# Kernel tuning notes

Hardware: AMD Instinct MI355X
Metric: run time of the kernel (lower is better)

Reference implementation:

```python
import jax, jax.numpy as jnp
import numpy as np

NUM_EXPERTS = 8

def setup_inputs() -> dict:
    key = jax.random.key(0)
    k1, k2, k3, k4, k5 = jax.random.split(key, 5)
    B, T, E, C = 4, 4096, NUM_EXPERTS, 512
    in_features, out_features = 1024, 4096
    i = in_features // E
    x = jax.random.normal(k1, (B, T, E, i), dtype=jnp.float32)
    weight = jax.random.normal(k2, (out_features, in_features), dtype=jnp.float32) * 0.02
    bias = jax.random.normal(k3, (out_features,), dtype=jnp.float32) * 0.02
    combine_array = jax.random.uniform(k4, (B, T, E, C), dtype=jnp.float32)
    dispatch_mask = jax.random.uniform(k5, (B, T, E, C), dtype=jnp.float32)
    return {"x": x, "weight": weight, "bias": bias,
            "combine_array": combine_array, "dispatch_mask": dispatch_mask}

def reference(x, weight, bias, combine_array, dispatch_mask):
    E = NUM_EXPERTS
    expert_in = weight.shape[1] // E
    # (O, E*i) -> (E, O, i), matching torch's weight.reshape(E, -1, i)
    w = weight.reshape(E, -1, expert_in)
    B = x.shape[0]
    xr = x.reshape(B, -1, E, expert_in)  # (B, T, E, i)
    # dispatch: gather tokens into per-expert buffers (B, E, C, i)
    xd = jnp.einsum('btei,btec->beci', xr, dispatch_mask)
    # homogeneous coords to fold bias into the per-expert matmul
    x_h = jnp.concatenate([xd, jnp.ones_like(xd[..., :1])], axis=-1)           # (B,E,C,i+1)
    b_h = jnp.broadcast_to(bias.reshape(1, -1, 1), (E, w.shape[1], 1))
    w_h = jnp.concatenate([w, b_h], axis=-1)                                    # (E,O,i+1)
    # per-expert grouped GEMM, then scatter-combine back to tokens
    y = jnp.einsum('beci,eoi->beco', x_h, w_h)                                  # (B,E,C,O)
    out = jnp.einsum('beco,btec->bto', y, combine_array)                        # (B,T,O)
    return out
```

## Files before the change

### kernel.cpp

```cpp
#include <hip/hip_runtime.h>
#include <hip/hip_bf16.h>

typedef short sx8 __attribute__((ext_vector_type(8)));
typedef short sx4 __attribute__((ext_vector_type(4)));
typedef float f32x4 __attribute__((ext_vector_type(4)));

__device__ __forceinline__ short f2bf(float f) {
  union { float f; unsigned u; } v; v.f = f;
  unsigned r = v.u + 0x7fffu + ((v.u >> 16) & 1u);
  return (short)(r >> 16);
}

#define GLL16(g, l)                                          \
  __builtin_amdgcn_global_load_lds(                          \
      (__attribute__((address_space(1))) void*)(g),          \
      (__attribute__((address_space(3))) void*)(l), 16, 0, 0)

__global__ __launch_bounds__(256) void w2t_kernel(const float* __restrict__ w,
                                                  short* __restrict__ W2T) {
  const long idx = (long)blockIdx.x * 256 + threadIdx.x;
  const int o = (int)(idx >> 10);
  const int r = (int)(idx & 1023);
  W2T[idx] = f2bf(w[((long)((r >> 7) * 4096 + o) << 7) + (r & 127)]);
}

__global__ __launch_bounds__(256) void tr_kernel(const float* __restrict__ src,
                                                 short* __restrict__ dst,
                                                 long sB0, long sB1, int SLD, int W) {
  __shared__ float tile[64][68];
  const int tid = threadIdx.x;
  const int bz = blockIdx.z;
  const long sBase = (long)(bz >> 3) * sB0 + (long)(bz & 7) * sB1;
  const long dBase = (long)bz * W * 4096;
  const int c0 = blockIdx.x * 64;
  const int t0 = blockIdx.y * 64;

#pragma unroll
  for (int it = 0; it < 4; ++it) {
    const int t = it * 16 + (tid >> 4);
    const int c4 = (tid & 15) * 4;
    f32x4 v = *(const f32x4*)(src + sBase + (long)(t0 + t) * SLD + c0 + c4);
    *(f32x4*)&tile[t][c4] = v;
  }
  __syncthreads();
#pragma unroll
  for (int it = 0; it < 4; ++it) {
    const int c = it * 16 + (tid >> 4);
    const int t4 = (tid & 15) * 4;
    sx4 o;
#pragma unroll
    for (int j = 0; j < 4; ++j) o[j] = f2bf(tile[t4 + j][c]);
    *(sx4*)(dst + dBase + (long)(c0 + c) * 4096 + t0 + t4) = o;
  }
}

__global__ __launch_bounds__(256, 4) void gemm_a_fused(const short* __restrict__ xT,
                                                       const float* __restrict__ disp,
                                                       float* __restrict__ P) {
  __shared__ short lA[128][40];
  __shared__ float sc[32][133];
  const int tid = threadIdx.x;
  const int c0 = blockIdx.x * 128;
  const int kb = blockIdx.y;
  const int bz = blockIdx.z;
  const long dBase = (long)(bz >> 3) * 16777216 + (long)(bz & 7) * 512;
  const long xBase = (long)bz * 524288;
  const long pBase = (long)kb * 2097152 + (long)bz * 65536;
  const int wid = tid >> 6, lane = tid & 63;
  const int wr = wid >> 1, wc = wid & 1;
  const int r0 = wr * 64, q0 = wc * 64;
  const int lrow = lane & 15, lk = (lane >> 4) << 3;

  f32x4 acc[4][4];
#pragma unroll
  for (int a = 0; a < 4; ++a)
#pragma unroll
    for (int b = 0; b < 4; ++b) acc[a][b] = (f32x4){0.f, 0.f, 0.f, 0.f};

  for (int kt0 = 0; kt0 < 1024; kt0 += 32) {
    const int kt = kb * 1024 + kt0;
#pragma unroll
    for (int it = 0; it < 2; ++it) {
      int idx = it * 256 + tid;
      int mr = idx >> 2, kc = (idx & 3) * 8;
      *(sx8*)&lA[mr][kc] = *(const sx8*)(xT + xBase + (long)mr * 4096 + kt + kc);
    }
#pragma unroll
    for (int it = 0; it < 4; ++it) {
      int idx = it * 256 + tid;
      int tr = idx >> 5, c4 = (idx & 31) * 4;
      f32x4 v = *(const f32x4*)(disp + dBase + (long)(kt + tr) * 4096 + c0 + c4);
      sc[tr][c4] = v[0]; sc[tr][c4 + 1] = v[1];
      sc[tr][c4 + 2] = v[2]; sc[tr][c4 + 3] = v[3];
    }
    __syncthreads();

    sx8 af[4], bfr[4];
#pragma unroll
    for (int mi = 0; mi < 4; ++mi) af[mi] = *(sx8*)&lA[r0 + mi * 16 + lrow][lk];
#pragma unroll
    for (int ni = 0; ni < 4; ++ni) {
      sx8 s;
      const int col = q0 + ni * 16 + lrow;
#pragma unroll
      for (int jj = 0; jj < 8; ++jj) s[jj] = f2bf(sc[lk + jj][col]);
      bfr[ni] = s;
    }
#pragma unroll
    for (int mi = 0; mi < 4; ++mi)
#pragma unroll
      for (int ni = 0; ni < 4; ++ni)
        acc[mi][ni] = __builtin_amdgcn_mfma_f32_16x16x32_bf16(af[mi], bfr[ni], acc[mi][ni], 0, 0, 0);
    __syncthreads();
  }

#pragma unroll
  for (int mi = 0; mi < 4; ++mi)
#pragma unroll
    for (int ni = 0; ni < 4; ++ni) {
      const int gnl = q0 + ni * 16 + lrow;
      const int gm = r0 + mi * 16 + ((lane >> 4) << 2);
      float* op = P + pBase + (long)gm * 512 + c0 + gnl;
      op[0] = acc[mi][ni][0];
      op[512] = acc[mi][ni][1];
      op[1024] = acc[mi][ni][2];
      op[1536] = acc[mi][ni][3];
    }
}

template <int BM, int BN, int ABF, int OBF, int EPI, int SACC, int SPLIT, int OT>
__global__ __launch_bounds__(256) void gemm_tpl(
    const void* __restrict__ Ap, const void* __restrict__ Bp, void* __restrict__ Op,
    int K,
    long aB0, long aB1, int aLd,
    long bB0, long bB1, int bLd,
    long oB0, long oB1, int oLd, long oSS,
    const float* __restrict__ bias, const float* __restrict__ Svec,
    float* __restrict__ Se) {
  constexpr int BK = 32;
  constexpr int LDK = BK + 8;
  constexpr int MI = BM / 32;
  constexpr int NI = BN / 32;
  constexpr int SITER = (BM * (BK / 4)) / 256;

  __shared__ short lA[BM][LDK];
  __shared__ short lB[BN][LDK];

  const int tid = threadIdx.x;
  const int bz = blockIdx.z;
  const long aBase = (long)(bz >> 3) * aB0 + (long)(bz & 7) * aB1;
  const long bBase = (long)(bz >> 3) * bB0 + (long)(bz & 7) * bB1;
  const int kb = (SPLIT > 1) ? blockIdx.y : 0;
  const long oBase = (long)(bz >> 3) * oB0 + (long)(bz & 7) * oB1 + (long)kb * oSS;
  const int m0 = blockIdx.x * BM;
  const int n0 = (SPLIT > 1) ? 0 : blockIdx.y * BN;
  const int kLo = kb * (K / SPLIT), kHi = kLo + K / SPLIT;

  const int wid = tid >> 6, lane = tid & 63;
  const int wr = wid >> 1, wc = wid & 1;
  const int r0 = wr * (BM / 2), c0 = wc * (BN / 2);
  const int lrow = lane & 15, lk = (lane >> 4) << 3;

  float ssum[SITER > 0 ? SITER : 1];
#pragma unroll
  for (int a = 0; a < SITER; ++a) ssum[a] = 0.f;

  f32x4 acc[MI][NI];
#pragma unroll
  for (int a = 0; a < MI; ++a)
#pragma unroll
    for (int b = 0; b < NI; ++b) acc[a][b] = (f32x4){0.f, 0.f, 0.f, 0.f};

  for (int kt = kLo; kt < kHi; kt += BK) {
    if constexpr (!ABF) {
      const float* A = (const float*)Ap + aBase + (long)m0 * aLd + kt;
      constexpr int QPR = BK / 4;
      constexpr int ITER = (BM * QPR) / 256;
#pragma unroll
      for (int it = 0; it < ITER; ++it) {
        int idx = it * 256 + tid;
        int mr = idx / QPR, kc = (idx % QPR) * 4;
        f32x4 v = *(const f32x4*)(A + (long)mr * aLd + kc);
        if constexpr (SACC) ssum[it] += v[0] + v[1] + v[2] + v[3];
        sx4 s;
#pragma unroll
        for (int j = 0; j < 4; ++j) s[j] = f2bf(v[j]);
        *(sx4*)&lA[mr][kc] = s;
      }
    } else {
      const short* A = (const short*)Ap + aBase + (long)m0 * aLd + kt;
      constexpr int CPR = BK / 8;
      constexpr int ITER = (BM * CPR) / 256;
#pragma unroll
      for (int it = 0; it < ITER; ++it) {
        int idx = it * 256 + tid;
        int mr = idx / CPR, kc = (idx % CPR) * 8;
        *(sx8*)&lA[mr][kc] = *(const sx8*)(A + (long)mr * aLd + kc);
      }
    }
    {
      const short* Bq = (const short*)Bp + bBase + (long)n0 * bLd + kt;
      constexpr int CPR = BK / 8;
      constexpr int ITER = (BN * CPR) / 256;
#pragma unroll
      for (int it = 0; it < ITER; ++it) {
        int idx = it * 256 + tid;
        int nr = idx / CPR, kc = (idx % CPR) * 8;
        *(sx8*)&lB[nr][kc] = *(const sx8*)(Bq + (long)nr * bLd + kc);
      }
    }
    __syncthreads();

    sx8 af[MI], bfr[NI];
#pragma unroll
    for (int mi = 0; mi < MI; ++mi) af[mi] = *(sx8*)&lA[r0 + mi * 16 + lrow][lk];
#pragma unroll
    for (int ni = 0; ni < NI; ++ni) bfr[ni] = *(sx8*)&lB[c0 + ni * 16 + lrow][lk];
#pragma unroll
    for (int mi = 0; mi < MI; ++mi)
#pragma unroll
      for (int ni = 0; ni < NI; ++ni)
        acc[mi][ni] = __builtin_amdgcn_mfma_f32_16x16x32_bf16(af[mi], bfr[ni], acc[mi][ni], 0, 0, 0);
    __syncthreads();
  }

  if constexpr (SACC) {
#pragma unroll
    for (int it = 0; it < SITER; ++it) {
      float s = ssum[it];
      s += __shfl_down(s, 4, 8);
      s += __shfl_down(s, 2, 8);
      s += __shfl_down(s, 1, 8);
      if ((tid & 7) == 0) {
        int mr = (it * 256 + tid) >> 3;
        Se[(long)(bz & 7) * 16384 + (long)(bz >> 3) * 4096 + m0 + mr] = s;
      }
    }
  }

  if constexpr (OT) {
#pragma unroll
    for (int mi = 0; mi < MI; ++mi) {
      const int gm_b = m0 + r0 + mi * 16 + ((lane >> 4) << 2);
#pragma unroll
      for (int ni = 0; ni < NI; ++ni) {
        const int gn = n0 + c0 + ni * 16 + lrow;
        *(f32x4*)((float*)Op + oBase + (long)gn * oLd + gm_b) = acc[mi][ni];
      }
    }
  } else {
#pragma unroll
    for (int mi = 0; mi < MI; ++mi) {
#pragma unroll
      for (int ni = 0; ni < NI; ++ni) {
        const int gn = n0 + c0 + ni * 16 + lrow;
        const int gm_b = m0 + r0 + mi * 16 + ((lane >> 4) << 2);
#pragma unroll
        for (int r = 0; r < 4; ++r) {
          const int gm = gm_b + r;
          float v = acc[mi][ni][r];
          if constexpr (EPI) v += bias[gn] * Svec[gm];
          const long addr = oBase + (long)gm * oLd + gn;
          if constexpr (OBF)
            ((short*)Op)[addr] = f2bf(v);
          else
            ((float*)Op)[addr] = v;
        }
      }
    }
  }
}

__global__ __launch_bounds__(256) void reduce_k(const float* __restrict__ P,
                                                short* __restrict__ xd) {
  const long i = ((long)blockIdx.x * 256 + threadIdx.x) * 4;
  f32x4 s = *(const f32x4*)(P + i);
#pragma unroll
  for (int sp = 1; sp < 4; ++sp) s += *(const f32x4*)(P + (long)sp * 2097152 + i);
  sx4 o;
#pragma unroll
  for (int j = 0; j < 4; ++j) o[j] = f2bf(s[j]);
  *(sx4*)&xd[i] = o;
}

__global__ __launch_bounds__(256) void ssum_k(const float* __restrict__ Se,
                                              float* __restrict__ S) {
  const int i = blockIdx.x * 256 + threadIdx.x;
  float s = 0.f;
#pragma unroll
  for (int e = 0; e < 8; ++e) s += Se[e * 16384 + i];
  S[i] = s;
}

#define BARX do { __asm__ __volatile__("" ::: "memory"); \
                  __builtin_amdgcn_s_barrier();           \
                  __asm__ __volatile__("" ::: "memory"); } while (0)

__global__ __launch_bounds__(512, 2) void gemm_c8(const short* __restrict__ Z,
                                                  const short* __restrict__ W,
                                                  float* __restrict__ Out,
                                                  const float* __restrict__ bias,
                                                  const float* __restrict__ Svec) {
  __shared__ short lAs[2 * 256 * 64];
  __shared__ short lBs[2 * 256 * 64];
  char* ldsA = (char*)lAs;
  char* ldsB = (char*)lBs;

  const int tid = threadIdx.x;
  const int lane = tid & 63, wid = tid >> 6;
  const int wr = wid >> 2, wc = wid & 3;
  const int lrow = lane & 15;

  const int sid = (blockIdx.x & 7) * 128 + (blockIdx.x >> 3);
  const int m0 = (sid >> 4) * 256;
  const int n0 = (sid & 15) * 256;

  const int rl = lane >> 3;
  const int csw = ((lane & 7) ^ rl) * 8;
  const short* srcA = Z + (long)(m0 + wid * 16 + rl) * 1024 + csw;
  const short* srcB = W + (long)(n0 + wid * 16 + rl) * 1024 + csw;
  const int cOff = wid * 2048;

#define STG_ALL(t) do {                                                          \
    long go = (long)(t) * 64;                                                    \
    int lo = (((t) & 1) << 15) + cOff;                                           \
    GLL16(srcA + go, ldsA + lo);                                                 \
    GLL16(srcA + go + 8192, ldsA + lo + 1024);                                   \
    GLL16(srcA + go + 131072, ldsA + lo + 16384);                                \
    GLL16(srcA + go + 131072 + 8192, ldsA + lo + 16384 + 1024);                  \
    GLL16(srcB + go, ldsB + lo);                                                 \
    GLL16(srcB + go + 8192, ldsB + lo + 1024);                                   \
    GLL16(srcB + go + 131072, ldsB + lo + 16384);                                \
    GLL16(srcB + go + 131072 + 8192, ldsB + lo + 16384 + 1024);                  \
  } while (0)

  const int xorv = (lane & 7) << 4;
  const int aBase = wr * 8192 + lrow * 128 + (lane >> 4) * 16;
  const int bBase = wc * 4096 + lrow * 128 + (lane >> 4) * 16;

  f32x4 acc[8][4];
#pragma unroll
  for (int a = 0; a < 8; ++a)
#pragma unroll
    for (int b = 0; b < 4; ++b) acc[a][b] = (f32x4){0.f, 0.f, 0.f, 0.f};

  sx8 af[4][2], bf0[2][2], bf1[2][2];

#define LOAD_A(qm, so) do {                                                    \
    _Pragma("unroll") for (int mi = 0; mi < 4; ++mi)                           \
    _Pragma("unroll") for (int ks = 0; ks < 2; ++ks) {                         \
      int bo = aBase + (qm) * 16384 + mi * 2048 + ks * 64;                     \
      af[mi][ks] = *(const sx8*)(ldsA + (so) + (bo ^ xorv));                   \
    }                                                                          \
  } while (0)
#define LOAD_B(dst, qn, so) do {                                               \
    _Pragma("unroll") for (int ni = 0; ni < 2; ++ni)                           \
    _Pragma("unroll") for (int ks = 0; ks < 2; ++ks) {                         \
      int bo = bBase + (qn) * 16384 + ni * 2048 + ks * 64;                     \
      dst[ni][ks] = *(const sx8*)(ldsB + (so) + (bo ^ xorv));                  \
    }                                                                          \
  } while (0)
#define MFMA32(qm) do {                                                        \
    __builtin_amdgcn_s_setprio(1);                                             \
    _Pragma("unroll") for (int mi = 0; mi < 4; ++mi)                           \
    _Pragma("unroll") for (int ni = 0; ni < 2; ++ni)                           \
    _Pragma("unroll") for (int ks = 0; ks < 2; ++ks) {                         \
      acc[(qm) * 4 + mi][ni] = __builtin_amdgcn_mfma_f32_16x16x32_bf16(        \
          af[mi][ks], bf0[ni][ks], acc[(qm) * 4 + mi][ni], 0, 0, 0);           \
      acc[(qm) * 4 + mi][2 + ni] = __builtin_amdgcn_mfma_f32_16x16x32_bf16(    \
          af[mi][ks], bf1[ni][ks], acc[(qm) * 4 + mi][2 + ni], 0, 0, 0);       \
    }                                                                          \
    __builtin_amdgcn_s_setprio(0);                                             \
  } while (0)

  STG_ALL(0);
  asm volatile("s_waitcnt vmcnt(0)" ::: "memory");
  BARX;

  for (int j = 0; j < 16; ++j) {
    const int so = (j & 1) << 15;
    LOAD_A(0, so);
    LOAD_B(bf0, 0, so);
    LOAD_B(bf1, 1, so);
    if (j < 15) STG_ALL(j + 1);
    MFMA32(0);
    LOAD_A(1, so);
    MFMA32(1);
    if (j < 15) asm volatile("s_waitcnt vmcnt(0)" ::: "memory");
    BARX;
  }

#pragma unroll
  for (int a = 0; a < 8; ++a) {
    const int gm = m0 + (a >> 2) * 128 + wr * 64 + (a & 3) * 16 + ((lane >> 4) << 2);
    const float s0 = Svec[gm], s1 = Svec[gm + 1], s2 = Svec[gm + 2], s3 = Svec[gm + 3];
#pragma unroll
    for (int b = 0; b < 4; ++b) {
      const int gn = n0 + (b >> 1) * 128 + wc * 32 + (b & 1) * 16 + lrow;
      const float bz = bias[gn];
      float* op = Out + (long)gm * 4096 + gn;
      op[0] = acc[a][b][0] + bz * s0;
      op[4096] = acc[a][b][1] + bz * s1;
      op[8192] = acc[a][b][2] + bz * s2;
      op[12288] = acc[a][b][3] + bz * s3;
    }
  }
#undef STG_ALL
#undef LOAD_A
#undef LOAD_B
#undef MFMA32
}

extern "C" void kernel_launch(void* const* d_in, const int* in_sizes, int n_in,
                              void* d_out, int out_size, void* d_ws, size_t ws_size,
                              hipStream_t stream) {
  const float* x        = (const float*)d_in[0];
  const float* weight   = (const float*)d_in[1];
  const float* bias     = (const float*)d_in[2];
  const float* combine  = (const float*)d_in[3];
  const float* dispatch = (const float*)d_in[4];
  float* out = (float*)d_out;

  char* ws = (char*)d_ws;
  short* W2T = (short*)ws;
  short* xdT = (short*)(ws + (8L << 20));
  float* S   = (float*)(ws + (12L << 20));
  float* Se  = (float*)(ws + (12L << 20) + 65536);
  short* xT  = (short*)(ws + (13L << 20));
  short* z2  = (short*)(ws + (13L << 20));
  float* P   = (float*)(ws + (45L << 20));

  w2t_kernel<<<dim3(16384), dim3(256), 0, stream>>>(weight, W2T);

  tr_kernel<<<dim3(2, 64, 32), dim3(256), 0, stream>>>(x, xT,
      4194304L, 128L, 1024, 128);

  gemm_a_fused<<<dim3(4, 4, 32), dim3(256), 0, stream>>>(xT, dispatch, P);

  reduce_k<<<dim3(2048), dim3(256), 0, stream>>>(P, xdT);

  gemm_tpl<128, 128, 0, 1, 0, 1, 1, 0><<<dim3(32, 1, 32), dim3(256), 0, stream>>>(
      combine, xdT, z2, 512,
      16777216L, 512L, 4096,
      524288L, 65536L, 512,
      4194304L, 128L, 1024, 0L,
      nullptr, nullptr, Se);

  ssum_k<<<dim3(64), dim3(256), 0, stream>>>(Se, S);

  gemm_c8<<<dim3(1024), dim3(512), 0, stream>>>(z2, W2T, out, bias, S);
}
```

Before: 363.4 us.

## Store split-K partials in bf16, convert dispatch tile once, remap gemm_c8 tiles per XCD

The dispatch GEMM now converts the dispatch tile to bf16 once when it is written to LDS, instead of converting every element on each fragment read. Its split-K partial outputs are stored as bf16, so the partial buffer and the reduction kernel move half the bytes. The final GEMM's block-to-tile mapping now gives each XCD a fixed pair of N columns, aiming for better L2 reuse of weight tiles. Rounding partial sums to bf16 before the reduction adds some numerical error.

Measured after the change: 343.9 us (median of 2 runs). 5.4% less time.

```diff
diff --git a/kernel.cpp b/kernel.cpp
--- a/kernel.cpp
+++ b/kernel.cpp
@@ -9,6 +9,11 @@
   union { float f; unsigned u; } v; v.f = f;
   unsigned r = v.u + 0x7fffu + ((v.u >> 16) & 1u);
   return (short)(r >> 16);
+}
+__device__ __forceinline__ float bf2f(short s) {
+  union { unsigned u; float f; } w;
+  w.u = ((unsigned)(unsigned short)s) << 16;
+  return w.f;
 }
 
 #define GLL16(g, l)                                          \
@@ -56,9 +61,9 @@
 
 __global__ __launch_bounds__(256, 4) void gemm_a_fused(const short* __restrict__ xT,
                                                        const float* __restrict__ disp,
-                                                       float* __restrict__ P) {
+                                                       short* __restrict__ P) {
   __shared__ short lA[128][40];
-  __shared__ float sc[32][133];
+  __shared__ short sc16[32][136];
   const int tid = threadIdx.x;
   const int c0 = blockIdx.x * 128;
   const int kb = blockIdx.y;
@@ -90,8 +95,10 @@
       int idx = it * 256 + tid;
       int tr = idx >> 5, c4 = (idx & 31) * 4;
       f32x4 v = *(const f32x4*)(disp + dBase + (long)(kt + tr) * 4096 + c0 + c4);
-      sc[tr][c4] = v[0]; sc[tr][c4 + 1] = v[1];
-      sc[tr][c4 + 2] = v[2]; sc[tr][c4 + 3] = v[3];
+      sx4 s;
+#pragma unroll
+      for (int j = 0; j < 4; ++j) s[j] = f2bf(v[j]);
+      *(sx4*)&sc16[tr][c4] = s;
     }
     __syncthreads();
 
@@ -103,7 +110,7 @@
       sx8 s;
       const int col = q0 + ni * 16 + lrow;
 #pragma unroll
-      for (int jj = 0; jj < 8; ++jj) s[jj] = f2bf(sc[lk + jj][col]);
+      for (int jj = 0; jj < 8; ++jj) s[jj] = sc16[lk + jj][col];
       bfr[ni] = s;
     }
 #pragma unroll
@@ -120,11 +127,11 @@
     for (int ni = 0; ni < 4; ++ni) {
       const int gnl = q0 + ni * 16 + lrow;
       const int gm = r0 + mi * 16 + ((lane >> 4) << 2);
-      float* op = P + pBase + (long)gm * 512 + c0 + gnl;
-      op[0] = acc[mi][ni][0];
-      op[512] = acc[mi][ni][1];
-      op[1024] = acc[mi][ni][2];
-      op[1536] = acc[mi][ni][3];
+      short* op = P + pBase + (long)gm * 512 + c0 + gnl;
+      op[0] = f2bf(acc[mi][ni][0]);
+      op[512] = f2bf(acc[mi][ni][1]);
+      op[1024] = f2bf(acc[mi][ni][2]);
+      op[1536] = f2bf(acc[mi][ni][3]);
     }
 }
 
@@ -271,12 +278,16 @@
   }
 }
 
-__global__ __launch_bounds__(256) void reduce_k(const float* __restrict__ P,
+__global__ __launch_bounds__(256) void reduce_k(const short* __restrict__ P,
                                                 short* __restrict__ xd) {
   const long i = ((long)blockIdx.x * 256 + threadIdx.x) * 4;
-  f32x4 s = *(const f32x4*)(P + i);
-#pragma unroll
-  for (int sp = 1; sp < 4; ++sp) s += *(const f32x4*)(P + (long)sp * 2097152 + i);
+  float s[4] = {0.f, 0.f, 0.f, 0.f};
+#pragma unroll
+  for (int sp = 0; sp < 4; ++sp) {
+    sx4 v = *(const sx4*)(P + (long)sp * 2097152 + i);
+#pragma unroll
+    for (int j = 0; j < 4; ++j) s[j] += bf2f(v[j]);
+  }
   sx4 o;
 #pragma unroll
   for (int j = 0; j < 4; ++j) o[j] = f2bf(s[j]);
@@ -311,9 +322,11 @@
   const int wr = wid >> 2, wc = wid & 3;
   const int lrow = lane & 15;
 
-  const int sid = (blockIdx.x & 7) * 128 + (blockIdx.x >> 3);
-  const int m0 = (sid >> 4) * 256;
-  const int n0 = (sid & 15) * 256;
+  const int bid = blockIdx.x;
+  const int xcd = bid & 7;
+  const int local = bid >> 3;
+  const int m0 = (local >> 1) * 256;
+  const int n0 = (xcd * 2 + (local & 1)) * 256;
 
   const int rl = lane >> 3;
   const int csw = ((lane & 7) ^ rl) * 8;
@@ -428,7 +441,7 @@
   float* Se  = (float*)(ws + (12L << 20) + 65536);
   short* xT  = (short*)(ws + (13L << 20));
   short* z2  = (short*)(ws + (13L << 20));
-  float* P   = (float*)(ws + (45L << 20));
+  short* P   = (short*)(ws + (45L << 20));
 
   w2t_kernel<<<dim3(16384), dim3(256), 0, stream>>>(weight, W2T);
 
```
